# Kernel tuning notes

Hardware: AMD Instinct MI355X
Metric: run time of the kernel (lower is better)

## Reference

```python
import jax, jax.numpy as jnp
import numpy as np

B, N, C = 8, 8192, 64
P, K = 2048, 16
C_IN = 2 * C + 6   # 134: concat(diff, center) of (feat ++ xyz)
H1, H2 = 64, 128
EPS = 1e-5


def setup_inputs() -> dict:
    key = jax.random.key(0)
    ks = jax.random.split(key, 16)
    inp = {
        "xyz": jax.random.normal(ks[0], (B, N, 3), dtype=jnp.float32),
        "feat": jax.random.normal(ks[1], (B, C, N), dtype=jnp.float32),
        # SharedMLP layer 1: 1x1 conv + BN(eval) + ReLU
        "W1": jax.random.normal(ks[2], (H1, C_IN), dtype=jnp.float32) * (1.0 / np.sqrt(C_IN)),
        "b1": jnp.zeros((H1,), dtype=jnp.float32),
        "g1": jax.random.uniform(ks[3], (H1,), minval=0.5, maxval=1.5, dtype=jnp.float32),
        "be1": jax.random.normal(ks[4], (H1,), dtype=jnp.float32) * 0.1,
        "m1": jax.random.normal(ks[5], (H1,), dtype=jnp.float32) * 0.1,
        "v1": jax.random.uniform(ks[6], (H1,), minval=0.5, maxval=1.5, dtype=jnp.float32),
        # SharedMLP layer 2
        "W2": jax.random.normal(ks[7], (H2, H1), dtype=jnp.float32) * (1.0 / np.sqrt(H1)),
        "b2": jnp.zeros((H2,), dtype=jnp.float32),
        "g2": jax.random.uniform(ks[8], (H2,), minval=0.5, maxval=1.5, dtype=jnp.float32),
        "be2": jax.random.normal(ks[9], (H2,), dtype=jnp.float32) * 0.1,
        "m2": jax.random.normal(ks[10], (H2,), dtype=jnp.float32) * 0.1,
        "v2": jax.random.uniform(ks[11], (H2,), minval=0.5, maxval=1.5, dtype=jnp.float32),
        "npoints": P,
    }
    return inp


def _mlp_layer(x, W, b, g, be, m, v):
    # x: [b,p,k,cin] -> 1x1 conv (einsum) + eval-mode BN + ReLU
    y = jnp.einsum("bpkc,oc->bpko", x, W) + b
    y = g * (y - m) * jax.lax.rsqrt(v + EPS) + be
    return jax.nn.relu(y)


def reference(xyz, feat, W1, b1, g1, be1, m1, v1, W2, b2, g2, be2, m2, v2, npoints):
    p = npoints
    # Range sampling: take first p points
    new_xyz = xyz[:, :p]                       # [b,p,3]
    feat_t = jnp.swapaxes(feat, 1, 2)          # [b,n,c]
    feat_x = jnp.concatenate([feat_t, xyz], axis=-1)   # [b,n,c+3] (use_xyz)
    new_feat_x = feat_x[:, :p]                 # [b,p,c+3]
    # KNN via squared euclidean distance, expanded form to avoid [b,p,n,3]
    sq_q = jnp.sum(new_xyz * new_xyz, axis=-1)           # [b,p]
    sq_r = jnp.sum(xyz * xyz, axis=-1)                   # [b,n]
    dots = jnp.einsum("bpd,bnd->bpn", new_xyz, xyz)      # [b,p,n]
    d2 = sq_q[:, :, None] + sq_r[:, None, :] - 2.0 * dots
    _, idx = jax.lax.top_k(-d2, K)             # [b,p,k] nearest (ascending dist)
    # Gather neighbor features: [b,p,k,c+3]
    knn_feat = jax.vmap(lambda f, i: f[i])(feat_x, idx)
    tiled = jnp.broadcast_to(new_feat_x[:, :, None, :], knn_feat.shape)
    edge = jnp.concatenate([knn_feat - tiled, tiled], axis=-1)  # [b,p,k,2c+6]
    h = _mlp_layer(edge, W1, b1, g1, be1, m1, v1)
    h = _mlp_layer(h, W2, b2, g2, be2, m2, v2)              # [b,p,k,H2]
    new_feat = jnp.swapaxes(jnp.max(h, axis=2), 1, 2)       # [b,H2,p]
    sample_idx = jnp.broadcast_to(jnp.arange(p, dtype=jnp.int32), (xyz.shape[0], p))
    return new_xyz, new_feat, sample_idx
```

## Files before the change

kernel.cpp:

```cpp
#include <hip/hip_runtime.h>
#include <hip/hip_bf16.h>

#define BB 8
#define NN 8192
#define CC 64
#define PP 2048
#define KK 16
#define H1 64
#define H2 128
#define K1PAD 160
#define K2PAD 72

typedef float  f32x4 __attribute__((ext_vector_type(4)));
typedef short  s16x8 __attribute__((ext_vector_type(8)));

#define OFF_FXT   0u
#define OFF_PTS4  17825792u
#define OFF_KNN   19922944u
#define OFF_W1P   20971520u
#define OFF_W2P   20992000u
#define OFF_C1    21010432u
#define OFF_C2    21010688u

#define FLTMAX 3.402823466e+38f

static __device__ __forceinline__ unsigned short bf16b(float v) {
    __hip_bfloat16 h = __float2bfloat16(v);
    return *reinterpret_cast<unsigned short*>(&h);
}
static __device__ __forceinline__ unsigned pk2(float a, float b) {
    return ((unsigned)bf16b(b) << 16) | (unsigned)bf16b(a);
}
#define LDS_FENCE() asm volatile("s_waitcnt lgkmcnt(0)" ::: "memory")

__global__ __launch_bounds__(512) void k1_prep(const float* __restrict__ xyz,
                                               const float* __restrict__ feat,
                                               float* __restrict__ fxt,
                                               float4* __restrict__ pts4,
                                               float* __restrict__ out0,
                                               float* __restrict__ out2) {
    __shared__ float tile[68][65];
    int b  = blockIdx.x >> 7;
    int n0 = (blockIdx.x & 127) * 64;
    int tx = threadIdx.x & 63, ty = threadIdx.x >> 6;
    for (int c = ty; c < 68; c += 8) {
        float v;
        if (c < 64)       v = feat[((size_t)b * 64 + c) * NN + n0 + tx];
        else if (c < 67)  v = xyz[((size_t)b * NN + n0 + tx) * 3 + (c - 64)];
        else              v = 0.f;
        tile[c][tx] = v;
    }
    __syncthreads();
    size_t base = ((size_t)b * NN + n0) * 68;
    for (int e = threadIdx.x; e < 64 * 68; e += 512) {
        int nl = e / 68, c = e - nl * 68;
        fxt[base + e] = tile[c][nl];
    }
    if (threadIdx.x < 64) {
        int n = n0 + threadIdx.x;
        float x = tile[64][threadIdx.x], y = tile[65][threadIdx.x], z = tile[66][threadIdx.x];
        pts4[(size_t)b * NN + n] = make_float4(x, y, z, x * x + y * y + z * z);
        if (n0 < PP) out2[b * PP + n] = (float)n;
    }
    if (n0 < PP) {
        for (int e = threadIdx.x; e < 64 * 3; e += 512) {
            int nl = e / 3, d = e - nl * 3;
            out0[((size_t)b * PP + n0 + nl) * 3 + d] = tile[64 + d][nl];
        }
    }
}

__global__ __launch_bounds__(1024, 2) void k2_knn(const float4* __restrict__ pts4,
                                                  int* __restrict__ knn,
                                                  const float* __restrict__ W1, const float* __restrict__ b1,
                                                  const float* __restrict__ g1, const float* __restrict__ be1,
                                                  const float* __restrict__ m1, const float* __restrict__ v1,
                                                  const float* __restrict__ W2, const float* __restrict__ b2,
                                                  const float* __restrict__ g2, const float* __restrict__ be2,
                                                  const float* __restrict__ m2, const float* __restrict__ v2,
                                                  unsigned short* __restrict__ w1p,
                                                  unsigned short* __restrict__ w2p,
                                                  float* __restrict__ c1, float* __restrict__ c2) {
    __shared__ float4 stage[8192];
    __shared__ float2 scratch[16][2][64];
    int lane = threadIdx.x & 63;
    int wv   = threadIdx.x >> 6;
    int b    = blockIdx.x >> 5;
    int q0   = (blockIdx.x & 31) * 64 + wv * 4;
    size_t pb = (size_t)b * NN;

    float4 qc = make_float4(0.f, 0.f, 0.f, 0.f);
    if (lane < 4) qc = pts4[pb + q0 + lane];
    float qx2 = -2.f * qc.x, qy2 = -2.f * qc.y, qz2 = -2.f * qc.z;
    float bx[4], by[4], bz[4];
#pragma unroll
    for (int q = 0; q < 4; ++q) {
        bx[q] = __shfl(qx2, q); by[q] = __shfl(qy2, q); bz[q] = __shfl(qz2, q);
    }

#pragma unroll
    for (int i = 0; i < 8; ++i) {
        int p = i * 1024 + threadIdx.x;
        float4 v = pts4[pb + p];
        int r = p >> 6, c = p & 63;
        stage[(r << 6) | ((c + (r >> 1)) & 63)] = v;
    }

    if (threadIdx.x < 77) {
        int i = blockIdx.x * 77 + threadIdx.x;
        if (i < 64 * K1PAD) {
            int n = i / K1PAD, c = i - n * K1PAD;
            float s = g1[n] * rsqrtf(v1[n] + 1e-5f);
            float val = 0.f;
            if (c < 67)                  val = W1[n * 134 + c] * s;
            else if (c >= 72 && c < 139) val = W1[n * 134 + (c - 5)] * s;
            w1p[i] = bf16b(val);
        } else if (i < 19456) {
            int j = i - 10240;
            int o = j / K2PAD, k = j - o * K2PAD;
            float s = g2[o] * rsqrtf(v2[o] + 1e-5f);
            w2p[j] = bf16b((k < 64) ? W2[o * 64 + k] * s : 0.f);
        } else if (i < 19520) {
            int l = i - 19456;
            float s = g1[l] * rsqrtf(v1[l] + 1e-5f);
            c1[l] = s * (b1[l] - m1[l]) + be1[l];
        } else if (i < 19648) {
            int p = i - 19520;
            float s = g2[p] * rsqrtf(v2[p] + 1e-5f);
            c2[p] = s * (b2[p] - m2[p]) + be2[p];
        }
    }
    __syncthreads();

    float m[4];
#pragma unroll
    for (int q = 0; q < 4; ++q) m[q] = FLTMAX;
#pragma unroll
    for (int rr = 0; rr < 2; ++rr) {
        int rowbase = (2 * lane + rr) << 6;
#pragma unroll
        for (int j8 = 0; j8 < 8; ++j8) {
            float4 cc[8];
#pragma unroll
            for (int i = 0; i < 8; ++i)
                cc[i] = stage[rowbase | ((j8 * 8 + i + lane) & 63)];
#pragma unroll
            for (int q = 0; q < 4; ++q) {
                float x = bx[q], y = by[q], z = bz[q];
#pragma unroll
                for (int i = 0; i < 8; i += 2) {
                    float e0 = fmaf(z, cc[i].z, fmaf(y, cc[i].y, fmaf(x, cc[i].x, cc[i].w)));
                    float e1 = fmaf(z, cc[i+1].z, fmaf(y, cc[i+1].y, fmaf(x, cc[i+1].x, cc[i+1].w)));
                    m[q] = fminf(fminf(m[q], e0), e1);
                }
            }
        }
    }

    float sv0 = m[0], sv1 = m[1], sv2 = m[2], sv3 = m[3];
#pragma unroll
    for (int k = 2; k <= 64; k <<= 1) {
#pragma unroll
        for (int j = k >> 1; j > 0; j >>= 1) {
            bool keepMin = (((lane & k) == 0) == ((lane & j) == 0));
            float p0 = __shfl_xor(sv0, j, 64);
            float p1 = __shfl_xor(sv1, j, 64);
            float p2 = __shfl_xor(sv2, j, 64);
            float p3 = __shfl_xor(sv3, j, 64);
            sv0 = keepMin ? fminf(sv0, p0) : fmaxf(sv0, p0);
            sv1 = keepMin ? fminf(sv1, p1) : fmaxf(sv1, p1);
            sv2 = keepMin ? fminf(sv2, p2) : fmaxf(sv2, p2);
            sv3 = keepMin ? fminf(sv3, p3) : fmaxf(sv3, p3);
        }
    }
    float T[4];
    T[0] = __shfl(sv0, 15, 64); T[1] = __shfl(sv1, 15, 64);
    T[2] = __shfl(sv2, 15, 64); T[3] = __shfl(sv3, 15, 64);

    unsigned long long below = (lane == 63) ? 0x7FFFFFFFFFFFFFFFull
                                            : ((1ull << lane) - 1ull);
#pragma unroll
    for (int pr = 0; pr < 4; pr += 2) {
        int Ms[2];
#pragma unroll
        for (int u = 0; u < 2; ++u) {
            int q = pr + u;
            float x = bx[q], y = by[q], z = bz[q], tq = T[q];
            unsigned long long rm = __ballot(m[q] <= tq);
            int cnt = 0;
            while (rm) {
                int sl = __ffsll((long long)rm) - 1; rm &= rm - 1;
                int phys = (lane + sl) & 63;
                float4 c0 = stage[((2 * sl) << 6) | phys];
                float4 c1v_ = stage[((2 * sl + 1) << 6) | phys];
                float e0 = fmaf(z, c0.z, fmaf(y, c0.y, fmaf(x, c0.x, c0.w)));
                float e1 = fmaf(z, c1v_.z, fmaf(y, c1v_.y, fmaf(x, c1v_.x, c1v_.w)));
                unsigned long long b0 = __ballot(e0 <= tq);
                if (e0 <= tq) {
                    int pos = cnt + __popcll(b0 & below);
                    if (pos < 64)
                        scratch[wv][u][pos] = make_float2(e0, __int_as_float(sl * 128 + lane));
                }
                cnt += __popcll(b0);
                unsigned long long b1 = __ballot(e1 <= tq);
                if (e1 <= tq) {
                    int pos = cnt + __popcll(b1 & below);
                    if (pos < 64)
                        scratch[wv][u][pos] = make_float2(e1, __int_as_float(sl * 128 + 64 + lane));
                }
                cnt += __popcll(b1);
            }
            Ms[u] = min(cnt, 64);
        }
        LDS_FENCE();
#pragma unroll
        for (int u = 0; u < 2; ++u) {
            int M = Ms[u];
            float2 own = scratch[wv][u][lane];
            float di = own.x; int ni = __float_as_int(own.y);
            int rank = 0;
            const float2* buf = &scratch[wv][u][0];
#pragma unroll 4
            for (int j = 0; j < M; ++j) {
                float2 e = buf[j];
                int nj = __float_as_int(e.y);
                rank += (e.x < di || (e.x == di && nj < ni)) ? 1 : 0;
            }
            if (lane < M && rank < 16)
                knn[((size_t)(b * PP + q0 + pr + u)) * KK + rank] = ni;
        }
        LDS_FENCE();
    }
}

__global__ __launch_bounds__(256, 2) void k3_mlp(const float* __restrict__ fxt,
                                                 const int* __restrict__ knn,
                                                 const unsigned short* __restrict__ w1p,
                                                 const unsigned short* __restrict__ w2p,
                                                 const float* __restrict__ c1,
                                                 const float* __restrict__ c2,
                                                 float* __restrict__ out1) {
    __shared__ __align__(16) char smem[4 * 5632];
    __shared__ float otile[16][132];
    __shared__ __align__(16) unsigned short w1lds[64 * 168];
    int lane = threadIdx.x & 63;
    int wv   = threadIdx.x >> 6;
    int b    = blockIdx.x & 7;
    int qg   = blockIdx.x >> 3;
    int qbase = qg * 16;
    char* seg = smem + wv * 5632;
    float4* sh_t4 = (float4*)(seg + 5120);
    unsigned* sh_tbd = (unsigned*)(seg + 5392);
    unsigned short* h1l = (unsigned short*)(seg);
    const float4* fx4 = (const float4*)fxt;

    int col = lane & 15, quad = lane >> 4;
    int r = lane >> 2, s = lane & 3;

    {
        const unsigned* src = (const unsigned*)w1p;
        unsigned* dst = (unsigned*)w1lds;
        for (int t = threadIdx.x; t < 5120; t += 256) {
            int row = t / 80, c = t - row * 80;
            dst[row * 84 + c] = src[t];
        }
    }

    s16x8 w2f[2][8];
#pragma unroll
    for (int ks = 0; ks < 2; ++ks)
#pragma unroll
        for (int nt = 0; nt < 8; ++nt)
            w2f[ks][nt] = *(const s16x8*)(w2p + (nt * 16 + col) * K2PAD + ks * 32 + quad * 8);
    float c1v[4], c2v[8];
#pragma unroll
    for (int nt = 0; nt < 4; ++nt) c1v[nt] = c1[nt * 16 + col];
#pragma unroll
    for (int nt = 0; nt < 8; ++nt) c2v[nt] = c2[nt * 16 + col];

    int idxAll = knn[((size_t)(b * PP + qbase + wv * 4)) * KK + lane];

    __syncthreads();

    float4 cc[2][5];
    float4 tv[2];

#define PREFETCH(buf, qi_) {                                                  \
        int q_ = qbase + wv * 4 + (qi_);                                      \
        tv[buf] = make_float4(0.f, 0.f, 0.f, 0.f);                            \
        if (lane < 17) tv[buf] = fx4[((size_t)b * NN + q_) * 17 + lane];      \
        int nidx_ = __shfl(idxAll, (qi_) * 16 + r, 64);                       \
        const float4* rowp_ = fx4 + ((size_t)b * NN + nidx_) * 17;            \
        cc[buf][0] = rowp_[s];      cc[buf][1] = rowp_[4 + s];                \
        cc[buf][2] = rowp_[8 + s];  cc[buf][3] = rowp_[12 + s];               \
        cc[buf][4] = rowp_[16]; }

    PREFETCH(0, 0);

#pragma unroll
    for (int qi = 0; qi < 4; ++qi) {
        int cur = qi & 1, nxt = cur ^ 1;
        if (lane < 17) {
            float4 v = tv[cur];
            sh_t4[lane] = v;
            sh_tbd[lane * 2]     = pk2(v.x, v.y);
            sh_tbd[lane * 2 + 1] = pk2(v.z, v.w);
        }
        LDS_FENCE();
        char* erow = seg + r * 320;
#pragma unroll
        for (int j = 0; j < 4; ++j) {
            int c4 = j * 4 + s;
            float4 v = cc[cur][j], t = sh_t4[c4];
            *(unsigned*)(erow + c4 * 8)     = pk2(v.x - t.x, v.y - t.y);
            *(unsigned*)(erow + c4 * 8 + 4) = pk2(v.z - t.z, v.w - t.w);
        }
        if (s == 0) {
            float4 v = cc[cur][4], t = sh_t4[16];
            *(unsigned*)(erow + 128) = pk2(v.x - t.x, v.y - t.y);
            *(unsigned*)(erow + 132) = pk2(v.z - t.z, v.w - t.w);
        }
        for (int j = s; j < 34; j += 4)
            *(unsigned*)(erow + 144 + j * 4) = sh_tbd[j];
#pragma unroll
        for (int i = lane; i < 192; i += 64) {
            int rr = i / 12, jj = i - rr * 12;
            int dw = (jj < 2) ? (34 + jj) : (68 + jj);
            *(unsigned*)(seg + rr * 320 + dw * 4) = 0u;
        }
        if (qi < 3) PREFETCH(nxt, qi + 1);
        LDS_FENCE();
        f32x4 acc1[4];
#pragma unroll
        for (int nt = 0; nt < 4; ++nt) acc1[nt] = (f32x4){0.f, 0.f, 0.f, 0.f};
#pragma unroll
        for (int ks = 0; ks < 5; ++ks) {
            s16x8 a = *(const s16x8*)(seg + col * 320 + ks * 64 + quad * 16);
#pragma unroll
            for (int nt = 0; nt < 4; ++nt) {
                s16x8 bf = *(const s16x8*)(w1lds + (nt * 16 + col) * 168 + ks * 32 + quad * 8);
                acc1[nt] = __builtin_amdgcn_mfma_f32_16x16x32_bf16(a, bf, acc1[nt], 0, 0, 0);
            }
        }
#pragma unroll
        for (int nt = 0; nt < 4; ++nt) {
#pragma unroll
            for (int rr = 0; rr < 4; ++rr) {
                float y = fmaxf(acc1[nt][rr] + c1v[nt], 0.f);
                h1l[(quad * 4 + rr) * K2PAD + nt * 16 + col] = bf16b(y);
            }
        }
        LDS_FENCE();
        f32x4 acc2[8];
#pragma unroll
        for (int nt = 0; nt < 8; ++nt) acc2[nt] = (f32x4){0.f, 0.f, 0.f, 0.f};
#pragma unroll
        for (int ks = 0; ks < 2; ++ks) {
            s16x8 a = *(const s16x8*)(seg + col * 144 + ks * 64 + quad * 16);
#pragma unroll
            for (int nt = 0; nt < 8; ++nt)
                acc2[nt] = __builtin_amdgcn_mfma_f32_16x16x32_bf16(a, w2f[ks][nt], acc2[nt], 0, 0, 0);
        }
#pragma unroll
        for (int nt = 0; nt < 8; ++nt) {
            float m0 = fmaxf(fmaxf(acc2[nt][0], acc2[nt][1]), fmaxf(acc2[nt][2], acc2[nt][3]));
            m0 = m0 + c2v[nt];
            m0 = fmaxf(m0, 0.f);
            m0 = fmaxf(m0, __shfl_xor(m0, 16, 64));
            m0 = fmaxf(m0, __shfl_xor(m0, 32, 64));
            if (quad == 0)
                otile[wv * 4 + qi][nt * 16 + col] = m0;
        }
        LDS_FENCE();
    }
    __syncthreads();
    for (int i = threadIdx.x; i < H2 * 16; i += 256) {
        int ch = i >> 4, q = i & 15;
        out1[((size_t)(b * H2 + ch)) * PP + qbase + q] = otile[q][ch];
    }
#undef PREFETCH
}

extern "C" void kernel_launch(void* const* d_in, const int* in_sizes, int n_in,
                              void* d_out, int out_size, void* d_ws, size_t ws_size,
                              hipStream_t stream) {
    const float* xyz  = (const float*)d_in[0];
    const float* feat = (const float*)d_in[1];
    const float* W1   = (const float*)d_in[2];
    const float* b1   = (const float*)d_in[3];
    const float* g1   = (const float*)d_in[4];
    const float* be1  = (const float*)d_in[5];
    const float* m1   = (const float*)d_in[6];
    const float* v1   = (const float*)d_in[7];
    const float* W2   = (const float*)d_in[8];
    const float* b2   = (const float*)d_in[9];
    const float* g2   = (const float*)d_in[10];
    const float* be2  = (const float*)d_in[11];
    const float* m2   = (const float*)d_in[12];
    const float* v2   = (const float*)d_in[13];

    char* ws = (char*)d_ws;
    float*          fxt  = (float*)(ws + OFF_FXT);
    float4*         pts4 = (float4*)(ws + OFF_PTS4);
    int*            knn  = (int*)(ws + OFF_KNN);
    unsigned short* w1p  = (unsigned short*)(ws + OFF_W1P);
    unsigned short* w2p  = (unsigned short*)(ws + OFF_W2P);
    float*          c1   = (float*)(ws + OFF_C1);
    float*          c2   = (float*)(ws + OFF_C2);

    float* out0 = (float*)d_out;
    float* out1 = out0 + (size_t)BB * PP * 3;
    float* out2 = out1 + (size_t)BB * H2 * PP;

    hipLaunchKernelGGL(k1_prep, dim3(1024), dim3(512), 0, stream,
                       xyz, feat, fxt, pts4, out0, out2);
    hipLaunchKernelGGL(k2_knn, dim3(256), dim3(1024), 0, stream, pts4, knn,
                       W1, b1, g1, be1, m1, v1, W2, b2, g2, be2, m2, v2,
                       w1p, w2p, c1, c2);
    hipLaunchKernelGGL(k3_mlp, dim3(1024), dim3(256), 0, stream,
                       fxt, knn, w1p, w2p, c1, c2, out1);
}
```

Before: 166.3 us.

## Store transposed feature table as packed bf16 and build edge rows from it

The prep kernel now writes the transposed feature+xyz table as packed bf16 pairs (72 channels, 36 dwords per point) instead of fp32 (68 floats). The MLP kernel gathers neighbor and center rows as uint4 vectors, computes the differences by unpacking the bf16 values and repacking, and copies the center half straight from LDS with wide stores. This halves gather traffic and the table's footprint and simplifies edge construction. The cost is that subtraction now uses values already rounded to bf16, which adds double-rounding error to the difference features.

```diff
diff --git a/kernel.cpp b/kernel.cpp
--- a/kernel.cpp
+++ b/kernel.cpp
@@ -31,19 +31,27 @@
 static __device__ __forceinline__ unsigned pk2(float a, float b) {
     return ((unsigned)bf16b(b) << 16) | (unsigned)bf16b(a);
 }
+static __device__ __forceinline__ unsigned dpk(unsigned v, unsigned t) {
+    float v0 = __uint_as_float(v << 16), v1 = __uint_as_float(v & 0xffff0000u);
+    float t0 = __uint_as_float(t << 16), t1 = __uint_as_float(t & 0xffff0000u);
+    return pk2(v0 - t0, v1 - t1);
+}
+static __device__ __forceinline__ uint4 dpk4(uint4 v, uint4 t) {
+    return make_uint4(dpk(v.x, t.x), dpk(v.y, t.y), dpk(v.z, t.z), dpk(v.w, t.w));
+}
 #define LDS_FENCE() asm volatile("s_waitcnt lgkmcnt(0)" ::: "memory")
 
 __global__ __launch_bounds__(512) void k1_prep(const float* __restrict__ xyz,
                                                const float* __restrict__ feat,
-                                               float* __restrict__ fxt,
+                                               unsigned* __restrict__ fxtb,
                                                float4* __restrict__ pts4,
                                                float* __restrict__ out0,
                                                float* __restrict__ out2) {
-    __shared__ float tile[68][65];
+    __shared__ float tile[72][65];
     int b  = blockIdx.x >> 7;
     int n0 = (blockIdx.x & 127) * 64;
     int tx = threadIdx.x & 63, ty = threadIdx.x >> 6;
-    for (int c = ty; c < 68; c += 8) {
+    for (int c = ty; c < 72; c += 8) {
         float v;
         if (c < 64)       v = feat[((size_t)b * 64 + c) * NN + n0 + tx];
         else if (c < 67)  v = xyz[((size_t)b * NN + n0 + tx) * 3 + (c - 64)];
@@ -51,10 +59,10 @@
         tile[c][tx] = v;
     }
     __syncthreads();
-    size_t base = ((size_t)b * NN + n0) * 68;
-    for (int e = threadIdx.x; e < 64 * 68; e += 512) {
-        int nl = e / 68, c = e - nl * 68;
-        fxt[base + e] = tile[c][nl];
+    size_t base = ((size_t)b * NN + n0) * 36;
+    for (int e = threadIdx.x; e < 64 * 36; e += 512) {
+        int nl = e / 36, c = e - nl * 36;
+        fxtb[base + e] = pk2(tile[2 * c][nl], tile[2 * c + 1][nl]);
     }
     if (threadIdx.x < 64) {
         int n = n0 + threadIdx.x;
@@ -233,7 +241,7 @@
     }
 }
 
-__global__ __launch_bounds__(256, 2) void k3_mlp(const float* __restrict__ fxt,
+__global__ __launch_bounds__(256, 2) void k3_mlp(const unsigned* __restrict__ fxtb,
                                                  const int* __restrict__ knn,
                                                  const unsigned short* __restrict__ w1p,
                                                  const unsigned short* __restrict__ w2p,
@@ -249,10 +257,9 @@
     int qg   = blockIdx.x >> 3;
     int qbase = qg * 16;
     char* seg = smem + wv * 5632;
-    float4* sh_t4 = (float4*)(seg + 5120);
-    unsigned* sh_tbd = (unsigned*)(seg + 5392);
+    uint4* sh_tc = (uint4*)(seg + 5120);
     unsigned short* h1l = (unsigned short*)(seg);
-    const float4* fx4 = (const float4*)fxt;
+    const uint4* fx4 = (const uint4*)fxtb;
 
     int col = lane & 15, quad = lane >> 4;
     int r = lane >> 2, s = lane & 3;
@@ -282,52 +289,40 @@
 
     __syncthreads();
 
-    float4 cc[2][5];
-    float4 tv[2];
+    uint4 cc[2][3];
+    uint4 tv[2];
 
 #define PREFETCH(buf, qi_) {                                                  \
         int q_ = qbase + wv * 4 + (qi_);                                      \
-        tv[buf] = make_float4(0.f, 0.f, 0.f, 0.f);                            \
-        if (lane < 17) tv[buf] = fx4[((size_t)b * NN + q_) * 17 + lane];      \
+        if (lane < 9) tv[buf] = fx4[((size_t)b * NN + q_) * 9 + lane];        \
         int nidx_ = __shfl(idxAll, (qi_) * 16 + r, 64);                       \
-        const float4* rowp_ = fx4 + ((size_t)b * NN + nidx_) * 17;            \
-        cc[buf][0] = rowp_[s];      cc[buf][1] = rowp_[4 + s];                \
-        cc[buf][2] = rowp_[8 + s];  cc[buf][3] = rowp_[12 + s];               \
-        cc[buf][4] = rowp_[16]; }
+        const uint4* rowp_ = fx4 + ((size_t)b * NN + nidx_) * 9;              \
+        cc[buf][0] = rowp_[s];                                                \
+        cc[buf][1] = rowp_[4 + s];                                            \
+        if (s == 0) cc[buf][2] = rowp_[8]; }
 
     PREFETCH(0, 0);
 
 #pragma unroll
     for (int qi = 0; qi < 4; ++qi) {
         int cur = qi & 1, nxt = cur ^ 1;
-        if (lane < 17) {
-            float4 v = tv[cur];
-            sh_t4[lane] = v;
-            sh_tbd[lane * 2]     = pk2(v.x, v.y);
-            sh_tbd[lane * 2 + 1] = pk2(v.z, v.w);
-        }
+        if (lane < 9) sh_tc[lane] = tv[cur];
         LDS_FENCE();
         char* erow = seg + r * 320;
-#pragma unroll
-        for (int j = 0; j < 4; ++j) {
-            int c4 = j * 4 + s;
-            float4 v = cc[cur][j], t = sh_t4[c4];
-            *(unsigned*)(erow + c4 * 8)     = pk2(v.x - t.x, v.y - t.y);
-            *(unsigned*)(erow + c4 * 8 + 4) = pk2(v.z - t.z, v.w - t.w);
-        }
-        if (s == 0) {
-            float4 v = cc[cur][4], t = sh_t4[16];
-            *(unsigned*)(erow + 128) = pk2(v.x - t.x, v.y - t.y);
-            *(unsigned*)(erow + 132) = pk2(v.z - t.z, v.w - t.w);
-        }
-        for (int j = s; j < 34; j += 4)
-            *(unsigned*)(erow + 144 + j * 4) = sh_tbd[j];
-#pragma unroll
-        for (int i = lane; i < 192; i += 64) {
-            int rr = i / 12, jj = i - rr * 12;
-            int dw = (jj < 2) ? (34 + jj) : (68 + jj);
-            *(unsigned*)(seg + rr * 320 + dw * 4) = 0u;
-        }
+        {
+            uint4 v = cc[cur][0], t = sh_tc[s];
+            *(uint4*)(erow + s * 16) = dpk4(v, t);
+            v = cc[cur][1]; t = sh_tc[4 + s];
+            *(uint4*)(erow + (4 + s) * 16) = dpk4(v, t);
+            if (s == 0) {
+                v = cc[cur][2]; t = sh_tc[8];
+                *(uint4*)(erow + 128) = dpk4(v, t);
+            }
+        }
+        for (int j = s; j < 9; j += 4)
+            *(uint4*)(erow + (9 + j) * 16) = sh_tc[j];
+        if (s < 2)
+            *(uint4*)(erow + (18 + s) * 16) = make_uint4(0u, 0u, 0u, 0u);
         if (qi < 3) PREFETCH(nxt, qi + 1);
         LDS_FENCE();
         f32x4 acc1[4];
@@ -400,7 +395,7 @@
     const float* v2   = (const float*)d_in[13];
 
     char* ws = (char*)d_ws;
-    float*          fxt  = (float*)(ws + OFF_FXT);
+    unsigned*       fxtb = (unsigned*)(ws + OFF_FXT);
     float4*         pts4 = (float4*)(ws + OFF_PTS4);
     int*            knn  = (int*)(ws + OFF_KNN);
     unsigned short* w1p  = (unsigned short*)(ws + OFF_W1P);
@@ -413,10 +408,10 @@
     float* out2 = out1 + (size_t)BB * H2 * PP;
 
     hipLaunchKernelGGL(k1_prep, dim3(1024), dim3(512), 0, stream,
-                       xyz, feat, fxt, pts4, out0, out2);
+                       xyz, feat, fxtb, pts4, out0, out2);
     hipLaunchKernelGGL(k2_knn, dim3(256), dim3(1024), 0, stream, pts4, knn,
                        W1, b1, g1, be1, m1, v1, W2, b2, g2, be2, m2, v2,
                        w1p, w2p, c1, c2);
     hipLaunchKernelGGL(k3_mlp, dim3(1024), dim3(256), 0, stream,
-                       fxt, knn, w1p, w2p, c1, c2, out1);
-}
+                       fxtb, knn, w1p, w2p, c1, c2, out1);
+}
```

Result: no change. 164.3 us (-1.2%).
